# Optimization experiments

Hardware: AMD Instinct MI355X
Metric: run time of the kernel (lower is better)

Reference implementation:

```python
import jax, jax.numpy as jnp
import numpy as np

NUM_NODES = 50000
D_IN = 256
D_OUT = 256
N_QUERIES = 128
PER_GROUP = 256            # edges per query group in the last step (> max_edges)
E1 = N_QUERIES * PER_GROUP # 32768
E0 = 32768
RATIO = 0.2                # ratio_update


def setup_inputs() -> dict:
    key = jax.random.key(0)
    ks = jax.random.split(key, 10)
    d4 = 4 * D_IN
    rng = np.random.default_rng(0)
    # last-step edges: col0 = query idx (sorted, equal-size groups), col6 = src, col7 = dst
    edges1 = np.zeros((E1, 8), np.int64)
    edges1[:, 0] = np.repeat(np.arange(N_QUERIES), PER_GROUP)
    edges1[:, 6] = rng.integers(0, NUM_NODES, E1)
    edges1[:, 7] = rng.integers(0, NUM_NODES, E1)
    # earlier-step edges
    edges0 = np.zeros((E0, 8), np.int64)
    edges0[:, 0] = rng.integers(0, N_QUERIES, E0)
    edges0[:, 6] = rng.integers(0, NUM_NODES, E0)
    edges0[:, 7] = rng.integers(0, NUM_NODES, E0)
    return {
        "visited_node_score": jax.random.uniform(ks[0], (NUM_NODES,), jnp.float32),
        "visited_node_representation": jax.random.normal(ks[1], (NUM_NODES, D_IN), jnp.float32),
        "selected_edges0": jnp.asarray(edges0),
        "selected_edges1": jnp.asarray(edges1),
        "rel_emb0": jax.random.normal(ks[2], (E0, D_IN), jnp.float32),
        "rel_emb1": jax.random.normal(ks[3], (E1, D_IN), jnp.float32),
        "query_src_ts_emb": jax.random.normal(ks[4], (N_QUERIES, D_IN), jnp.float32),
        "query_rel_emb": jax.random.normal(ks[5], (N_QUERIES, D_IN), jnp.float32),
        "Wq": jax.random.normal(ks[6], (d4, d4), jnp.float32) * np.sqrt(2.0 / d4),
        "Wk": jax.random.normal(ks[7], (d4, d4), jnp.float32) * np.sqrt(2.0 / d4),
        "Wl": jax.random.normal(ks[8], (D_OUT, D_IN), jnp.float32) * np.sqrt(2.0 / (D_IN + D_OUT)),
        "bl": jnp.zeros((D_OUT,), jnp.float32),
        "max_edges": 64,
    }


def _att_score(edges, node_repr, rel, qst_tab, qr_tab, Wq, Wk):
    # G3: sum(Q(cat(vi,rel,qst,qr)) * K(cat(vj,rel,qst,qr)), -1) per edge
    q, src, dst = edges[:, 0], edges[:, 6], edges[:, 7]
    qst, qr = qst_tab[q], qr_tab[q]
    left = jnp.concatenate([node_repr[src], rel, qst, qr], axis=-1)   # [E, 4d]
    right = jnp.concatenate([node_repr[dst], rel, qst, qr], axis=-1)  # [E, 4d]
    return jnp.sum((left @ Wq.T) * (right @ Wk.T), axis=-1)          # [E]


def _seg_softmax(logits, seg, n):
    m = jax.ops.segment_max(logits, seg, num_segments=n)
    e = jnp.exp(logits - m[seg])
    s = jax.ops.segment_sum(e, seg, num_segments=n)
    return e / s[seg]


def _update_repr(edges, node_repr, w, ratio):
    # sparse mm: out[src] += (1-ratio)*w_e*repr[dst]; + identity for non-src rows, + ratio*repr for src rows
    src, dst = edges[:, 6], edges[:, 7]
    n = node_repr.shape[0]
    agg = jax.ops.segment_sum(((1.0 - ratio) * w)[:, None] * node_repr[dst], src, num_segments=n)
    is_src = jnp.zeros((n,), bool).at[src].set(True)
    diag = jnp.where(is_src, ratio, 1.0)
    return agg + diag[:, None] * node_repr


def reference(visited_node_score, visited_node_representation, selected_edges0,
              selected_edges1, rel_emb0, rel_emb1, query_src_ts_emb, query_rel_emb,
              Wq, Wk, Wl, bl, max_edges):
    n = visited_node_representation.shape[0]
    nq = query_src_ts_emb.shape[0]
    pg = selected_edges1.shape[0] // nq
    # attention on last step's edges
    logits = _att_score(selected_edges1, visited_node_representation, rel_emb1,
                        query_src_ts_emb, query_rel_emb, Wq, Wk)
    src1 = selected_edges1[:, 6]
    src_score = visited_node_score[src1]
    soft = _seg_softmax(logits, src1, n)
    target = soft * src_score
    # per-query-group top-k pruning (each group has pg > k edges)
    _, ti = jax.lax.top_k(target.reshape(nq, pg), max_edges)  # [nq, k]
    orig_indices = (ti + (jnp.arange(nq) * pg)[:, None]).reshape(-1)
    pruned_edges = selected_edges1[orig_indices]
    pruned_src_score = src_score[orig_indices]
    pruned_soft = soft[orig_indices]
    # sparse scatter-aggregation of scores onto dst (col 7)
    updated_node_score = jax.ops.segment_sum(pruned_soft * pruned_src_score,
                                             pruned_edges[:, 7], num_segments=n)
    node_repr = _update_repr(pruned_edges, visited_node_representation, pruned_soft, RATIO)
    # back-propagate representations through the earlier step
    tl = _att_score(selected_edges0, node_repr, rel_emb0, query_src_ts_emb, query_rel_emb, Wq, Wk)
    ts = _seg_softmax(tl, selected_edges0[:, 6], n)
    node_repr = _update_repr(selected_edges0, node_repr, ts, RATIO)
    # bypass_forward: LeakyReLU(Linear(.))
    node_repr = jax.nn.leaky_relu(node_repr @ Wl.T + bl)
    return (updated_node_score, node_repr, pruned_edges, orig_indices)
```

## Files before the change

kernel.cpp:

```cpp
#include <hip/hip_runtime.h>

#define NN 50000
#define D 256
#define NQ 128
#define PG 256
#define NE 32768
#define ME 64
#define BCAP 32
#define KDIM 256
#define NKT 8

typedef _Float16 f16;
typedef __attribute__((ext_vector_type(4))) _Float16 f16x4;
typedef __attribute__((ext_vector_type(8))) _Float16 f16x8;
typedef __attribute__((ext_vector_type(4))) float f32x4;

#define MFMA16(a,b,c) __builtin_amdgcn_mfma_f32_16x16x32_f16(a,b,c,0,0,0)

__device__ __forceinline__ f16x8 zero8(){
  f16x8 z;
#pragma unroll
  for (int i=0;i<8;++i) z[i] = (_Float16)0.f;
  return z;
}
__device__ __forceinline__ unsigned fenc(float f){
  unsigned b = __float_as_uint(f);
  return (b & 0x80000000u) ? ~b : (b | 0x80000000u);
}
__device__ __forceinline__ float fdec(unsigned u){
  unsigned b = (u & 0x80000000u) ? (u & 0x7fffffffu) : ~u;
  return __uint_as_float(b);
}

template<int EPI>
__global__ __launch_bounds__(256) void hgemm(const f16* __restrict__ Ah, const f16* __restrict__ Al,
                                             int Mrows,
                                             const f16* __restrict__ Bh, const f16* __restrict__ Bl,
                                             float* __restrict__ C, int ldc,
                                             const float* __restrict__ bias)
{
  __shared__ f16 AsH[128*40], AsL[128*40], BsH[128*40], BsL[128*40];
  const int tid = threadIdx.x;
  const int rb = blockIdx.x*128, cb = blockIdx.y*128;
  const int row = tid >> 1, ko = (tid & 1)*16;
  const bool aok = (rb + row) < Mrows;
  const int lane = tid & 63, wv = tid >> 6;
  const int qr = (wv & 1)*64, qc = (wv >> 1)*64;
  const int lm = lane & 15, qd = lane >> 4;

  const f16* gAh = Ah + (size_t)(rb+row)*KDIM + ko;
  const f16* gAl = Al + (size_t)(rb+row)*KDIM + ko;
  const f16* gBh = Bh + (size_t)(cb+row)*KDIM + ko;
  const f16* gBl = Bl + (size_t)(cb+row)*KDIM + ko;

  f16x8 pah0=zero8(), pah1=zero8(), pal0=zero8(), pal1=zero8();
  f16x8 pbh0, pbh1, pbl0, pbl1;
  if (aok){ pah0 = *(const f16x8*)gAh; pah1 = *(const f16x8*)(gAh+8);
            pal0 = *(const f16x8*)gAl; pal1 = *(const f16x8*)(gAl+8); }
  pbh0 = *(const f16x8*)gBh; pbh1 = *(const f16x8*)(gBh+8);
  pbl0 = *(const f16x8*)gBl; pbl1 = *(const f16x8*)(gBl+8);

  f32x4 acc[4][4];
#pragma unroll
  for (int t=0;t<4;++t)
#pragma unroll
    for (int u=0;u<4;++u)
#pragma unroll
      for (int r=0;r<4;++r) acc[t][u][r] = 0.f;

  const int wbase = row*40 + ko;
  for (int kt = 0; kt < NKT; ++kt){
    __syncthreads();
    *(f16x8*)(AsH + wbase) = pah0; *(f16x8*)(AsH + wbase + 8) = pah1;
    *(f16x8*)(AsL + wbase) = pal0; *(f16x8*)(AsL + wbase + 8) = pal1;
    *(f16x8*)(BsH + wbase) = pbh0; *(f16x8*)(BsH + wbase + 8) = pbh1;
    *(f16x8*)(BsL + wbase) = pbl0; *(f16x8*)(BsL + wbase + 8) = pbl1;
    __syncthreads();
    if (kt+1 < NKT){
      const int k0 = (kt+1)*32;
      if (aok){ pah0 = *(const f16x8*)(gAh + k0); pah1 = *(const f16x8*)(gAh + k0 + 8);
                pal0 = *(const f16x8*)(gAl + k0); pal1 = *(const f16x8*)(gAl + k0 + 8); }
      pbh0 = *(const f16x8*)(gBh + k0); pbh1 = *(const f16x8*)(gBh + k0 + 8);
      pbl0 = *(const f16x8*)(gBl + k0); pbl1 = *(const f16x8*)(gBl + k0 + 8);
    }
    f16x8 fah[4], fal[4], fbh[4], fbl[4];
#pragma unroll
    for (int t=0;t<4;++t){
      int off = (qr + t*16 + lm)*40 + qd*8;
      fah[t] = *(const f16x8*)(AsH + off);
      fal[t] = *(const f16x8*)(AsL + off);
    }
#pragma unroll
    for (int u=0;u<4;++u){
      int off = (qc + u*16 + lm)*40 + qd*8;
      fbh[u] = *(const f16x8*)(BsH + off);
      fbl[u] = *(const f16x8*)(BsL + off);
    }
#pragma unroll
    for (int t=0;t<4;++t)
#pragma unroll
      for (int u=0;u<4;++u){
        acc[t][u] = MFMA16(fah[t], fbh[u], acc[t][u]);
        acc[t][u] = MFMA16(fah[t], fbl[u], acc[t][u]);
        acc[t][u] = MFMA16(fal[t], fbh[u], acc[t][u]);
      }
  }
#pragma unroll
  for (int t=0;t<4;++t){
#pragma unroll
    for (int u=0;u<4;++u){
      int col = cb + qc + u*16 + lm;
      f32x4 v = acc[t][u];
#pragma unroll
      for (int r=0;r<4;++r){
        int rg = rb + qr + t*16 + qd*4 + r;
        if (rg < Mrows){
          float x = v[r];
          if (EPI==1){ x += bias[col]; x = x > 0.f ? x : 0.01f*x; }
          C[(size_t)rg*ldc + col] = x;
        }
      }
    }
  }
}

__global__ __launch_bounds__(256) void hgemm_rel(const f16* __restrict__ Ah, const f16* __restrict__ Al,
                                                 const f16* __restrict__ Bh, const f16* __restrict__ Bl,
                                                 const int* __restrict__ edges,
                                                 const float* __restrict__ H,
                                                 const float* __restrict__ Rel,
                                                 float* __restrict__ logits)
{
  __shared__ f16 AsH[128*40], AsL[128*40], BsH[128*40], BsL[128*40];
  __shared__ int sIdx[128];
  const int tid = threadIdx.x;
  const int rb = blockIdx.x*128, cb = blockIdx.y*128;
  const int sec = blockIdx.y >> 1;
  const int row = tid >> 1, ko = (tid & 1)*16;
  const int lane = tid & 63, wv = tid >> 6;
  const int qr = (wv & 1)*64, qc = (wv >> 1)*64;
  const int lm = lane & 15, qd = lane >> 4;

  if (tid < 128){
    int e = rb + tid;
    sIdx[tid] = (sec==0) ? edges[(size_t)e*8+6] : (sec==1 ? edges[(size_t)e*8+7] : 0);
  }

  const f16* gAh = Ah + (size_t)(rb+row)*KDIM + ko;
  const f16* gAl = Al + (size_t)(rb+row)*KDIM + ko;
  const f16* gBh = Bh + (size_t)(cb+row)*KDIM + ko;
  const f16* gBl = Bl + (size_t)(cb+row)*KDIM + ko;

  f16x8 pah0 = *(const f16x8*)gAh, pah1 = *(const f16x8*)(gAh+8);
  f16x8 pal0 = *(const f16x8*)gAl, pal1 = *(const f16x8*)(gAl+8);
  f16x8 pbh0 = *(const f16x8*)gBh, pbh1 = *(const f16x8*)(gBh+8);
  f16x8 pbl0 = *(const f16x8*)gBl, pbl1 = *(const f16x8*)(gBl+8);

  f32x4 acc[4][4];
#pragma unroll
  for (int t=0;t<4;++t)
#pragma unroll
    for (int u=0;u<4;++u)
#pragma unroll
      for (int r=0;r<4;++r) acc[t][u][r] = 0.f;

  const int wbase = row*40 + ko;
  for (int kt = 0; kt < NKT; ++kt){
    __syncthreads();
    *(f16x8*)(AsH + wbase) = pah0; *(f16x8*)(AsH + wbase + 8) = pah1;
    *(f16x8*)(AsL + wbase) = pal0; *(f16x8*)(AsL + wbase + 8) = pal1;
    *(f16x8*)(BsH + wbase) = pbh0; *(f16x8*)(BsH + wbase + 8) = pbh1;
    *(f16x8*)(BsL + wbase) = pbl0; *(f16x8*)(BsL + wbase + 8) = pbl1;
    __syncthreads();
    if (kt+1 < NKT){
      const int k0 = (kt+1)*32;
      pah0 = *(const f16x8*)(gAh + k0); pah1 = *(const f16x8*)(gAh + k0 + 8);
      pal0 = *(const f16x8*)(gAl + k0); pal1 = *(const f16x8*)(gAl + k0 + 8);
      pbh0 = *(const f16x8*)(gBh + k0); pbh1 = *(const f16x8*)(gBh + k0 + 8);
      pbl0 = *(const f16x8*)(gBl + k0); pbl1 = *(const f16x8*)(gBl + k0 + 8);
    }
    f16x8 fah[4], fal[4], fbh[4], fbl[4];
#pragma unroll
    for (int t=0;t<4;++t){
      int off = (qr + t*16 + lm)*40 + qd*8;
      fah[t] = *(const f16x8*)(AsH + off);
      fal[t] = *(const f16x8*)(AsL + off);
    }
#pragma unroll
    for (int u=0;u<4;++u){
      int off = (qc + u*16 + lm)*40 + qd*8;
      fbh[u] = *(const f16x8*)(BsH + off);
      fbl[u] = *(const f16x8*)(BsL + off);
    }
#pragma unroll
    for (int t=0;t<4;++t)
#pragma unroll
      for (int u=0;u<4;++u){
        acc[t][u] = MFMA16(fah[t], fbh[u], acc[t][u]);
        acc[t][u] = MFMA16(fah[t], fbl[u], acc[t][u]);
        acc[t][u] = MFMA16(fal[t], fbh[u], acc[t][u]);
      }
  }
  const int cbase = ((blockIdx.y & 1)*128) + qc + lm;
#pragma unroll
  for (int t=0;t<4;++t){
#pragma unroll
    for (int r=0;r<4;++r){
      int lrow = qr + t*16 + qd*4 + r;
      int e = rb + lrow;
      const float* xb = (sec==2) ? (Rel + (size_t)e*256)
                                 : (H + (size_t)sIdx[lrow]*256);
      float p = acc[t][0][r]*xb[cbase]
              + acc[t][1][r]*xb[cbase+16]
              + acc[t][2][r]*xb[cbase+32]
              + acc[t][3][r]*xb[cbase+48];
      p += __shfl_xor(p, 1); p += __shfl_xor(p, 2);
      p += __shfl_xor(p, 4); p += __shfl_xor(p, 8);
      if (lm == 0) atomicAdd(logits + e, p);
    }
  }
}

__global__ void split_f16(const float* __restrict__ X, f16* __restrict__ Xh,
                          f16* __restrict__ Xl, int n)
{
  int i = (blockIdx.x*256 + threadIdx.x)*4;
  if (i >= n) return;
  float4 v = *(const float4*)(X+i);
  f16x4 h, l;
  h[0]=(_Float16)v.x; h[1]=(_Float16)v.y; h[2]=(_Float16)v.z; h[3]=(_Float16)v.w;
  l[0]=(_Float16)(v.x-(float)h[0]); l[1]=(_Float16)(v.y-(float)h[1]);
  l[2]=(_Float16)(v.z-(float)h[2]); l[3]=(_Float16)(v.w-(float)h[3]);
  *(f16x4*)(Xh+i)=h; *(f16x4*)(Xl+i)=l;
}

__global__ void build_bt_mhh(const float* __restrict__ M, f16* __restrict__ Bh, f16* __restrict__ Bl)
{
  int idx = blockIdx.x*256 + threadIdx.x;
  int n = idx >> 8, k = idx & 255;
  float v = M[(size_t)k*1024 + n];
  _Float16 h = (_Float16)v;
  Bh[idx] = h; Bl[idx] = (_Float16)(v - (float)h);
}

__global__ void build_bt_wcat(const float* __restrict__ M, f16* __restrict__ Bh, f16* __restrict__ Bl)
{
  int idx = blockIdx.x*256 + threadIdx.x;
  int j = idx >> 8, k = idx & 255;
  float v;
  if (j < 256)      v = M[(size_t)j*1024 + 256 + k];
  else if (j < 512) v = M[(size_t)(256+k)*1024 + (j-256)];
  else              v = M[(size_t)(256 + j-512)*1024 + 256 + k];
  _Float16 h = (_Float16)v;
  Bh[idx] = h; Bl[idx] = (_Float16)(v - (float)h);
}

__global__ __launch_bounds__(256) void gemm_tn_split(const float* __restrict__ A,
                                                     const float* __restrict__ B,
                                                     double* __restrict__ Cpart)
{
  __shared__ float As[16][68];
  __shared__ float Bs[16][68];
  const int tid = threadIdx.x;
  const int rb = blockIdx.x * 64, cb = blockIdx.y * 64;
  const int z  = blockIdx.z;
  const int ty = tid >> 4, tx = tid & 15;
  const int aj = tid >> 4, akk = (tid & 15) << 2;
  double acc[4][4] = {};
  const int jbeg = z * 256, jend = jbeg + 256;
  for (int j0 = jbeg; j0 < jend; j0 += 16) {
    float4 av = *(const float4*)(A + (size_t)(j0+aj)*1024 + rb + akk);
    As[aj][akk+0]=av.x; As[aj][akk+1]=av.y; As[aj][akk+2]=av.z; As[aj][akk+3]=av.w;
    float4 bv = *(const float4*)(B + (size_t)(j0+aj)*1024 + cb + akk);
    Bs[aj][akk+0]=bv.x; Bs[aj][akk+1]=bv.y; Bs[aj][akk+2]=bv.z; Bs[aj][akk+3]=bv.w;
    __syncthreads();
#pragma unroll
    for (int jj=0; jj<16; ++jj){
      float a0=As[jj][ty*4+0],a1=As[jj][ty*4+1],a2=As[jj][ty*4+2],a3=As[jj][ty*4+3];
      float b0=Bs[jj][tx*4+0],b1=Bs[jj][tx*4+1],b2=Bs[jj][tx*4+2],b3=Bs[jj][tx*4+3];
      acc[0][0]+=(double)a0*b0; acc[0][1]+=(double)a0*b1; acc[0][2]+=(double)a0*b2; acc[0][3]+=(double)a0*b3;
      acc[1][0]+=(double)a1*b0; acc[1][1]+=(double)a1*b1; acc[1][2]+=(double)a1*b2; acc[1][3]+=(double)a1*b3;
      acc[2][0]+=(double)a2*b0; acc[2][1]+=(double)a2*b1; acc[2][2]+=(double)a2*b2; acc[2][3]+=(double)a2*b3;
      acc[3][0]+=(double)a3*b0; acc[3][1]+=(double)a3*b1; acc[3][2]+=(double)a3*b2; acc[3][3]+=(double)a3*b3;
    }
    __syncthreads();
  }
  double* Cz = Cpart + (size_t)z * 1048576;
#pragma unroll
  for (int i=0;i<4;++i)
#pragma unroll
    for (int j=0;j<4;++j)
      Cz[(size_t)(rb+ty*4+i)*1024 + cb+tx*4+j] = acc[i][j];
}

__global__ void reduce_m(const double* __restrict__ P, float* __restrict__ Mout)
{
  int i = blockIdx.x*256 + threadIdx.x;
  Mout[i] = (float)(P[i] + P[i+1048576] + P[i+2097152] + P[i+3145728]);
}

__global__ __launch_bounds__(256) void query_tables(const float* __restrict__ M,
    const float* __restrict__ qst, const float* __restrict__ qr,
    float* __restrict__ qt1, float* __restrict__ qt2, float* __restrict__ qw,
    float* __restrict__ qc)
{
  int q = blockIdx.x, t = threadIdx.x;
  __shared__ float g[512];
  __shared__ float red[256];
  g[t]       = qst[(size_t)q*256 + t];
  g[t + 256] = qr [(size_t)q*256 + t];
  __syncthreads();
  float s1=0.f, s2=0.f, sw=0.f, v1=0.f, v2=0.f;
  for (int k=0;k<512;++k){
    float gk = g[k];
    s1 += M[(size_t)t*1024 + 512 + k] * gk;
    s2 += M[(size_t)(512+k)*1024 + t] * gk;
    sw += (M[(size_t)(256+t)*1024 + 512 + k] +
           M[(size_t)(512+k)*1024 + 256 + t]) * gk;
    v1 += M[(size_t)(512+k)*1024 + 512 + t] * gk;
    v2 += M[(size_t)(512+k)*1024 + 768 + t] * gk;
  }
  qt1[(size_t)q*256+t]=s1; qt2[(size_t)q*256+t]=s2; qw[(size_t)q*256+t]=sw;
  red[t] = v1*g[t] + v2*g[t+256];
  __syncthreads();
  for (int s=128; s>0; s>>=1){
    if (t < s) red[t] += red[t+s];
    __syncthreads();
  }
  if (t==0) qc[q] = red[0];
}

__global__ __launch_bounds__(256) void slim_logits(const int* __restrict__ edges,
    const float* __restrict__ H, const float* __restrict__ U,
    const float* __restrict__ Rel,
    const float* __restrict__ qt1, const float* __restrict__ qt2,
    const float* __restrict__ qw, const float* __restrict__ qc,
    float* __restrict__ logits)
{
  int lane = threadIdx.x & 63;
  int e = blockIdx.x*4 + (threadIdx.x >> 6);
  int q   = edges[(size_t)e*8 + 0];
  int src = edges[(size_t)e*8 + 6];
  int dst = edges[(size_t)e*8 + 7];
  const float4* hs = (const float4*)(H   + (size_t)src*256);
  const float4* hd = (const float4*)(H   + (size_t)dst*256);
  const float4* us = (const float4*)(U   + (size_t)src*256);
  const float4* rl = (const float4*)(Rel + (size_t)e*256);
  const float4* t1 = (const float4*)(qt1 + (size_t)q*256);
  const float4* t2 = (const float4*)(qt2 + (size_t)q*256);
  const float4* w4 = (const float4*)(qw  + (size_t)q*256);
  float4 a, b, c;
  float s = 0.f;
  a = hd[lane]; b = us[lane]; c = t2[lane];
  s += a.x*(b.x+c.x) + a.y*(b.y+c.y) + a.z*(b.z+c.z) + a.w*(b.w+c.w);
  a = hs[lane]; c = t1[lane];
  s += a.x*c.x + a.y*c.y + a.z*c.z + a.w*c.w;
  a = rl[lane]; c = w4[lane];
  s += a.x*c.x + a.y*c.y + a.z*c.z + a.w*c.w;
#pragma unroll
  for (int off=32; off>0; off>>=1) s += __shfl_down(s, off);
  if (lane==0) logits[e] = s + qc[q];
}

__global__ void segmax_k(const int* __restrict__ edges, const float* __restrict__ logits,
                         unsigned* __restrict__ menc, int nE)
{
  int e = blockIdx.x*256 + threadIdx.x; if (e >= nE) return;
  atomicMax(menc + edges[(size_t)e*8+6], fenc(logits[e]));
}
__global__ void segexp_k(const int* __restrict__ edges, const float* __restrict__ logits,
                         const unsigned* __restrict__ menc, float* __restrict__ ebuf,
                         float* __restrict__ ssum, int nE)
{
  int e = blockIdx.x*256 + threadIdx.x; if (e >= nE) return;
  int s = edges[(size_t)e*8+6];
  float ex = expf(logits[e] - fdec(menc[s]));
  ebuf[e] = ex;
  atomicAdd(ssum + s, ex);
}
template<int TGT>
__global__ void segsoft_k(const int* __restrict__ edges, const float* __restrict__ ebuf,
                          const float* __restrict__ ssum, float* __restrict__ soft,
                          const float* __restrict__ score, float* __restrict__ target, int nE)
{
  int e = blockIdx.x*256 + threadIdx.x; if (e >= nE) return;
  int s = edges[(size_t)e*8+6];
  float so = ebuf[e] / ssum[s];
  soft[e] = so;
  if (TGT) target[e] = so * score[s];
}

__global__ __launch_bounds__(256) void topk_k(const float* __restrict__ target,
    const float* __restrict__ soft, const int* __restrict__ edges1,
    float* __restrict__ out0, float* __restrict__ out2, float* __restrict__ out3,
    int* __restrict__ p_src, int* __restrict__ p_dst, float* __restrict__ p_w)
{
  int qb = blockIdx.x, t = threadIdx.x;
  __shared__ float v[256];
  __shared__ int   ix[256];
  v[t] = target[(size_t)qb*256 + t];
  ix[t] = t;
  __syncthreads();
  for (int k=2; k<=256; k<<=1){
    for (int j=k>>1; j>0; j>>=1){
      int ixj = t ^ j;
      if (ixj > t){
        float va=v[t], vb=v[ixj]; int ia=ix[t], ib=ix[ixj];
        bool dir  = ((t & k) == 0);
        bool l_ab = (va > vb) || (va == vb && ia < ib);
        bool sw   = dir ? (!l_ab) : l_ab;
        if (sw){ v[t]=vb; v[ixj]=va; ix[t]=ib; ix[ixj]=ia; }
      }
      __syncthreads();
    }
  }
  if (t < 64){
    int oi = qb*256 + ix[t];
    int o  = qb*64 + t;
    out3[o] = (float)oi;
#pragma unroll
    for (int c2=0;c2<8;++c2) out2[(size_t)o*8 + c2] = (float)edges1[(size_t)oi*8 + c2];
    int s_ = edges1[(size_t)oi*8+6], d_ = edges1[(size_t)oi*8+7];
    p_src[o] = s_; p_dst[o] = d_; p_w[o] = soft[oi];
    atomicAdd(out0 + d_, v[t]);
  }
}

__global__ void bucket_fill(const int* __restrict__ srcarr, int stride, int n,
                            int* __restrict__ counts, int* __restrict__ bucket,
                            int* __restrict__ over, int* __restrict__ n_over)
{
  int e = blockIdx.x*256 + threadIdx.x; if (e >= n) return;
  int s = srcarr[(size_t)e*stride];
  int pos = atomicAdd(counts + s, 1);
  if (pos < BCAP) bucket[(size_t)s*BCAP + pos] = e;
  else { int oi = atomicAdd(n_over, 1); over[oi] = e; }
}

__global__ __launch_bounds__(256) void fused_update(const int* __restrict__ counts,
    const int* __restrict__ bucket, const int* __restrict__ dstarr, int dstride,
    const float* __restrict__ w, const float* __restrict__ Hin, float* __restrict__ Hout)
{
  int lane = threadIdx.x & 63;
  int n = blockIdx.x*4 + (threadIdx.x >> 6);
  if (n >= NN) return;
  int cnt = counts[n];
  float fac = cnt > 0 ? 0.2f : 1.0f;
  float4 h = ((const float4*)(Hin + (size_t)n*256))[lane];
  float4 acc = make_float4(fac*h.x, fac*h.y, fac*h.z, fac*h.w);
  int m = cnt < BCAP ? cnt : BCAP;
  for (int i=0;i<m;++i){
    int e = bucket[(size_t)n*BCAP + i];
    int d = dstarr[(size_t)e*dstride];
    float f = 0.8f * w[e];
    float4 vv = ((const float4*)(Hin + (size_t)d*256))[lane];
    acc.x += f*vv.x; acc.y += f*vv.y; acc.z += f*vv.z; acc.w += f*vv.w;
  }
  ((float4*)(Hout + (size_t)n*256))[lane] = acc;
}

__global__ __launch_bounds__(256) void over_k(const int* __restrict__ over,
    const int* __restrict__ n_over,
    const int* __restrict__ srcarr, int sstride,
    const int* __restrict__ dstarr, int dstride,
    const float* __restrict__ w, const float* __restrict__ Hin, float* __restrict__ Hout)
{
  int lane = threadIdx.x & 63;
  int i = blockIdx.x*4 + (threadIdx.x >> 6);
  if (i >= *n_over) return;
  int e = over[i];
  int s = srcarr[(size_t)e*sstride], d = dstarr[(size_t)e*dstride];
  float f = 0.8f * w[e];
  float4 vv = ((const float4*)(Hin + (size_t)d*256))[lane];
  float* o = Hout + (size_t)s*256 + lane*4;
  atomicAdd(o+0, f*vv.x); atomicAdd(o+1, f*vv.y);
  atomicAdd(o+2, f*vv.z); atomicAdd(o+3, f*vv.w);
}

extern "C" void kernel_launch(void* const* d_in, const int* in_sizes, int n_in,
                              void* d_out, int out_size, void* d_ws, size_t ws_size,
                              hipStream_t stream)
{
  const float* score = (const float*)d_in[0];
  const float* H0    = (const float*)d_in[1];
  const int*   edges0= (const int*)d_in[2];
  const int*   edges1= (const int*)d_in[3];
  const float* rel0  = (const float*)d_in[4];
  const float* rel1  = (const float*)d_in[5];
  const float* qst   = (const float*)d_in[6];
  const float* qr    = (const float*)d_in[7];
  const float* Wq    = (const float*)d_in[8];
  const float* Wk    = (const float*)d_in[9];
  const float* Wl    = (const float*)d_in[10];
  const float* bl    = (const float*)d_in[11];
  (void)in_sizes; (void)n_in; (void)out_size; (void)ws_size;

  float* out0 = (float*)d_out;
  float* out1 = out0 + NN;
  float* out2 = out1 + (size_t)NN*D;
  float* out3 = out2 + (size_t)NQ*ME*8;

  float* ws     = (float*)d_ws;
  float* Mbuf   = ws;
  float* qt1    = ws + 1048576;
  float* qt2    = ws + 1081344;
  float* qw     = ws + 1114112;
  float* qc     = ws + 1146880;
  float* logits = ws + 1147008;
  float* ebuf   = ws + 1179776;
  float* soft   = ws + 1212544;
  float* target = ws + 1245312;
  unsigned* menc= (unsigned*)(ws + 1278080);
  float* ssum   = ws + 1328080;
  int* p_src    = (int*)(ws + 1378080);
  int* p_dst    = (int*)(ws + 1386272);
  float* p_w    = ws + 1394464;
  float* U      = ws + 1402880;
  float* Hnew   = ws + 14202880;
  float* SCR    = ws + 27002880;
  int* counts = (int*)SCR;
  int* n_over = (int*)(SCR + 50000);
  int* over   = (int*)(SCR + 50056);
  int* bucket = (int*)(SCR + 100000);
  float* P0   = SCR + 2000000;
  f16* Ah = (f16*)P0;
  f16* Al = (f16*)(P0 + 6400000);
  f16* Rh = (f16*)(P0 + 12800000);
  f16* Rl = (f16*)(P0 + 16994304);
  f16* mhh_h  = (f16*)(P0 + 21200000);
  f16* mhh_l  = (f16*)(P0 + 21232768);
  f16* wcat_h = (f16*)(P0 + 21265536);
  f16* wcat_l = (f16*)(P0 + 21363840);
  f16* wl_h   = (f16*)(P0 + 21462144);
  f16* wl_l   = (f16*)(P0 + 21494912);
  double* Mpart = (double*)P0;
  float* Hpre = U;

  hipMemsetAsync(out0, 0, (size_t)NN*4, stream);
  hipMemsetAsync(menc, 0, (size_t)NN*4, stream);
  hipMemsetAsync(ssum, 0, (size_t)NN*4, stream);

  gemm_tn_split<<<dim3(16,16,4), 256, 0, stream>>>(Wq, Wk, Mpart);
  reduce_m<<<4096, 256, 0, stream>>>(Mpart, Mbuf);
  query_tables<<<NQ, 256, 0, stream>>>(Mbuf, qst, qr, qt1, qt2, qw, qc);
  build_bt_mhh<<<256, 256, 0, stream>>>(Mbuf, mhh_h, mhh_l);
  build_bt_wcat<<<768, 256, 0, stream>>>(Mbuf, wcat_h, wcat_l);
  split_f16<<<64, 256, 0, stream>>>(Wl, wl_h, wl_l, 65536);

  split_f16<<<12500, 256, 0, stream>>>(H0, Ah, Al, NN*256);
  hgemm<0><<<dim3(391,2), 256, 0, stream>>>(Ah, Al, NN, mhh_h, mhh_l, U, 256, nullptr);
  slim_logits<<<NE/4, 256, 0, stream>>>(edges1, H0, U, rel1, qt1, qt2, qw, qc, logits);
  split_f16<<<8192, 256, 0, stream>>>(rel1, Rh, Rl, NE*256);
  hgemm_rel<<<dim3(256,6), 256, 0, stream>>>(Rh, Rl, wcat_h, wcat_l, edges1, H0, rel1, logits);

  segmax_k<<<NE/256, 256, 0, stream>>>(edges1, logits, menc, NE);
  segexp_k<<<NE/256, 256, 0, stream>>>(edges1, logits, menc, ebuf, ssum, NE);
  segsoft_k<1><<<NE/256, 256, 0, stream>>>(edges1, ebuf, ssum, soft, score, target, NE);

  topk_k<<<NQ, 256, 0, stream>>>(target, soft, edges1, out0, out2, out3, p_src, p_dst, p_w);

  hipMemsetAsync(counts, 0, (size_t)NN*4, stream);
  hipMemsetAsync(n_over, 0, 4, stream);
  bucket_fill<<<(NQ*ME+255)/256, 256, 0, stream>>>(p_src, 1, NQ*ME, counts, bucket, over, n_over);
  fused_update<<<(NN+3)/4, 256, 0, stream>>>(counts, bucket, p_dst, 1, p_w, H0, Hnew);
  over_k<<<(NQ*ME)/4, 256, 0, stream>>>(over, n_over, p_src, 1, p_dst, 1, p_w, H0, Hnew);

  hipMemsetAsync(menc, 0, (size_t)NN*4, stream);
  hipMemsetAsync(ssum, 0, (size_t)NN*4, stream);

  split_f16<<<12500, 256, 0, stream>>>(Hnew, Ah, Al, NN*256);
  hgemm<0><<<dim3(391,2), 256, 0, stream>>>(Ah, Al, NN, mhh_h, mhh_l, U, 256, nullptr);
  slim_logits<<<NE/4, 256, 0, stream>>>(edges0, Hnew, U, rel0, qt1, qt2, qw, qc, logits);
  split_f16<<<8192, 256, 0, stream>>>(rel0, Rh, Rl, NE*256);
  hgemm_rel<<<dim3(256,6), 256, 0, stream>>>(Rh, Rl, wcat_h, wcat_l, edges0, Hnew, rel0, logits);

  segmax_k<<<NE/256, 256, 0, stream>>>(edges0, logits, menc, NE);
  segexp_k<<<NE/256, 256, 0, stream>>>(edges0, logits, menc, ebuf, ssum, NE);
  segsoft_k<0><<<NE/256, 256, 0, stream>>>(edges0, ebuf, ssum, soft, nullptr, nullptr, NE);

  hipMemsetAsync(counts, 0, (size_t)NN*4, stream);
  hipMemsetAsync(n_over, 0, 4, stream);
  bucket_fill<<<NE/256, 256, 0, stream>>>(edges0 + 6, 8, NE, counts, bucket, over, n_over);
  fused_update<<<(NN+3)/4, 256, 0, stream>>>(counts, bucket, edges0 + 7, 8, soft, Hnew, Hpre);
  over_k<<<NE/4, 256, 0, stream>>>(over, n_over, edges0 + 6, 8, edges0 + 7, 8, soft, Hnew, Hpre);

  split_f16<<<12500, 256, 0, stream>>>(Hpre, Ah, Al, NN*256);
  hgemm<1><<<dim3(391,2), 256, 0, stream>>>(Ah, Al, NN, wl_h, wl_l, out1, 256, bl);
}
```

Measured before the change: 739.2 us.

## Fuse f16 hi/lo split into GEMM loads and restructure query-table precompute

The GEMM kernels now read fp32 activations directly and split them into f16 high/low parts while staging into shared memory. This removes the five standalone split_f16 passes over the 50000x256 and 32768x256 matrices and their round trips through global memory. Separately, the per-query table computation moves from a serial 512-step loop per thread into a gather kernel plus a small tiled fp32 GEMM and a dot-product kernel. The Wq/Wk product split-K is widened from 4 to 8 partitions. The trade is extra conversion work inside the GEMM mainloop, twice the fp32 bytes per A load, and more small kernel launches.

```diff
diff --git a/kernel.cpp b/kernel.cpp
--- a/kernel.cpp
+++ b/kernel.cpp
@@ -17,12 +17,6 @@
 
 #define MFMA16(a,b,c) __builtin_amdgcn_mfma_f32_16x16x32_f16(a,b,c,0,0,0)
 
-__device__ __forceinline__ f16x8 zero8(){
-  f16x8 z;
-#pragma unroll
-  for (int i=0;i<8;++i) z[i] = (_Float16)0.f;
-  return z;
-}
 __device__ __forceinline__ unsigned fenc(float f){
   unsigned b = __float_as_uint(f);
   return (b & 0x80000000u) ? ~b : (b | 0x80000000u);
@@ -31,9 +25,18 @@
   unsigned b = (u & 0x80000000u) ? (u & 0x7fffffffu) : ~u;
   return __uint_as_float(b);
 }
+__device__ __forceinline__ void split8(float4 a, float4 b, f16x8& h, f16x8& l){
+  float v[8] = {a.x,a.y,a.z,a.w,b.x,b.y,b.z,b.w};
+#pragma unroll
+  for (int i=0;i<8;++i){
+    _Float16 hh = (_Float16)v[i];
+    h[i] = hh;
+    l[i] = (_Float16)(v[i] - (float)hh);
+  }
+}
 
 template<int EPI>
-__global__ __launch_bounds__(256) void hgemm(const f16* __restrict__ Ah, const f16* __restrict__ Al,
+__global__ __launch_bounds__(256) void hgemm(const float* __restrict__ A,
                                              int Mrows,
                                              const f16* __restrict__ Bh, const f16* __restrict__ Bl,
                                              float* __restrict__ C, int ldc,
@@ -45,18 +48,17 @@
   const int row = tid >> 1, ko = (tid & 1)*16;
   const bool aok = (rb + row) < Mrows;
   const int lane = tid & 63, wv = tid >> 6;
-  const int qr = (wv & 1)*64, qc = (wv >> 1)*64;
+  const int qrw = (wv & 1)*64, qcw = (wv >> 1)*64;
   const int lm = lane & 15, qd = lane >> 4;
 
-  const f16* gAh = Ah + (size_t)(rb+row)*KDIM + ko;
-  const f16* gAl = Al + (size_t)(rb+row)*KDIM + ko;
+  const float* gA = A + (size_t)(rb+row)*KDIM + ko;
   const f16* gBh = Bh + (size_t)(cb+row)*KDIM + ko;
   const f16* gBl = Bl + (size_t)(cb+row)*KDIM + ko;
 
-  f16x8 pah0=zero8(), pah1=zero8(), pal0=zero8(), pal1=zero8();
+  float4 pa0=make_float4(0.f,0.f,0.f,0.f), pa1=pa0, pa2=pa0, pa3=pa0;
   f16x8 pbh0, pbh1, pbl0, pbl1;
-  if (aok){ pah0 = *(const f16x8*)gAh; pah1 = *(const f16x8*)(gAh+8);
-            pal0 = *(const f16x8*)gAl; pal1 = *(const f16x8*)(gAl+8); }
+  if (aok){ pa0 = *(const float4*)gA;     pa1 = *(const float4*)(gA+4);
+            pa2 = *(const float4*)(gA+8); pa3 = *(const float4*)(gA+12); }
   pbh0 = *(const f16x8*)gBh; pbh1 = *(const f16x8*)(gBh+8);
   pbl0 = *(const f16x8*)gBl; pbl1 = *(const f16x8*)(gBl+8);
 
@@ -71,28 +73,32 @@
   const int wbase = row*40 + ko;
   for (int kt = 0; kt < NKT; ++kt){
     __syncthreads();
-    *(f16x8*)(AsH + wbase) = pah0; *(f16x8*)(AsH + wbase + 8) = pah1;
-    *(f16x8*)(AsL + wbase) = pal0; *(f16x8*)(AsL + wbase + 8) = pal1;
-    *(f16x8*)(BsH + wbase) = pbh0; *(f16x8*)(BsH + wbase + 8) = pbh1;
-    *(f16x8*)(BsL + wbase) = pbl0; *(f16x8*)(BsL + wbase + 8) = pbl1;
+    {
+      f16x8 h0,h1,l0,l1;
+      split8(pa0,pa1,h0,l0); split8(pa2,pa3,h1,l1);
+      *(f16x8*)(AsH + wbase) = h0; *(f16x8*)(AsH + wbase + 8) = h1;
+      *(f16x8*)(AsL + wbase) = l0; *(f16x8*)(AsL + wbase + 8) = l1;
+      *(f16x8*)(BsH + wbase) = pbh0; *(f16x8*)(BsH + wbase + 8) = pbh1;
+      *(f16x8*)(BsL + wbase) = pbl0; *(f16x8*)(BsL + wbase + 8) = pbl1;
+    }
     __syncthreads();
     if (kt+1 < NKT){
       const int k0 = (kt+1)*32;
-      if (aok){ pah0 = *(const f16x8*)(gAh + k0); pah1 = *(const f16x8*)(gAh + k0 + 8);
-                pal0 = *(const f16x8*)(gAl + k0); pal1 = *(const f16x8*)(gAl + k0 + 8); }
+      if (aok){ pa0 = *(const float4*)(gA + k0);     pa1 = *(const float4*)(gA + k0 + 4);
+                pa2 = *(const float4*)(gA + k0 + 8); pa3 = *(const float4*)(gA + k0 + 12); }
       pbh0 = *(const f16x8*)(gBh + k0); pbh1 = *(const f16x8*)(gBh + k0 + 8);
       pbl0 = *(const f16x8*)(gBl + k0); pbl1 = *(const f16x8*)(gBl + k0 + 8);
     }
     f16x8 fah[4], fal[4], fbh[4], fbl[4];
 #pragma unroll
     for (int t=0;t<4;++t){
-      int off = (qr + t*16 + lm)*40 + qd*8;
+      int off = (qrw + t*16 + lm)*40 + qd*8;
       fah[t] = *(const f16x8*)(AsH + off);
       fal[t] = *(const f16x8*)(AsL + off);
     }
 #pragma unroll
     for (int u=0;u<4;++u){
-      int off = (qc + u*16 + lm)*40 + qd*8;
+      int off = (qcw + u*16 + lm)*40 + qd*8;
       fbh[u] = *(const f16x8*)(BsH + off);
       fbl[u] = *(const f16x8*)(BsL + off);
     }
@@ -109,11 +115,11 @@
   for (int t=0;t<4;++t){
 #pragma unroll
     for (int u=0;u<4;++u){
-      int col = cb + qc + u*16 + lm;
+      int col = cb + qcw + u*16 + lm;
       f32x4 v = acc[t][u];
 #pragma unroll
       for (int r=0;r<4;++r){
-        int rg = rb + qr + t*16 + qd*4 + r;
+        int rg = rb + qrw + t*16 + qd*4 + r;
         if (rg < Mrows){
           float x = v[r];
           if (EPI==1){ x += bias[col]; x = x > 0.f ? x : 0.01f*x; }
@@ -124,7 +130,7 @@
   }
 }
 
-__global__ __launch_bounds__(256) void hgemm_rel(const f16* __restrict__ Ah, const f16* __restrict__ Al,
+__global__ __launch_bounds__(256) void hgemm_rel(const float* __restrict__ A,
                                                  const f16* __restrict__ Bh, const f16* __restrict__ Bl,
                                                  const int* __restrict__ edges,
                                                  const float* __restrict__ H,
@@ -138,7 +144,7 @@
   const int sec = blockIdx.y >> 1;
   const int row = tid >> 1, ko = (tid & 1)*16;
   const int lane = tid & 63, wv = tid >> 6;
-  const int qr = (wv & 1)*64, qc = (wv >> 1)*64;
+  const int qrw = (wv & 1)*64, qcw = (wv >> 1)*64;
   const int lm = lane & 15, qd = lane >> 4;
 
   if (tid < 128){
@@ -146,13 +152,12 @@
     sIdx[tid] = (sec==0) ? edges[(size_t)e*8+6] : (sec==1 ? edges[(size_t)e*8+7] : 0);
   }
 
-  const f16* gAh = Ah + (size_t)(rb+row)*KDIM + ko;
-  const f16* gAl = Al + (size_t)(rb+row)*KDIM + ko;
+  const float* gA = A + (size_t)(rb+row)*KDIM + ko;
   const f16* gBh = Bh + (size_t)(cb+row)*KDIM + ko;
   const f16* gBl = Bl + (size_t)(cb+row)*KDIM + ko;
 
-  f16x8 pah0 = *(const f16x8*)gAh, pah1 = *(const f16x8*)(gAh+8);
-  f16x8 pal0 = *(const f16x8*)gAl, pal1 = *(const f16x8*)(gAl+8);
+  float4 pa0 = *(const float4*)gA,     pa1 = *(const float4*)(gA+4);
+  float4 pa2 = *(const float4*)(gA+8), pa3 = *(const float4*)(gA+12);
   f16x8 pbh0 = *(const f16x8*)gBh, pbh1 = *(const f16x8*)(gBh+8);
   f16x8 pbl0 = *(const f16x8*)gBl, pbl1 = *(const f16x8*)(gBl+8);
 
@@ -167,28 +172,32 @@
   const int wbase = row*40 + ko;
   for (int kt = 0; kt < NKT; ++kt){
     __syncthreads();
-    *(f16x8*)(AsH + wbase) = pah0; *(f16x8*)(AsH + wbase + 8) = pah1;
-    *(f16x8*)(AsL + wbase) = pal0; *(f16x8*)(AsL + wbase + 8) = pal1;
-    *(f16x8*)(BsH + wbase) = pbh0; *(f16x8*)(BsH + wbase + 8) = pbh1;
-    *(f16x8*)(BsL + wbase) = pbl0; *(f16x8*)(BsL + wbase + 8) = pbl1;
+    {
+      f16x8 h0,h1,l0,l1;
+      split8(pa0,pa1,h0,l0); split8(pa2,pa3,h1,l1);
+      *(f16x8*)(AsH + wbase) = h0; *(f16x8*)(AsH + wbase + 8) = h1;
+      *(f16x8*)(AsL + wbase) = l0; *(f16x8*)(AsL + wbase + 8) = l1;
+      *(f16x8*)(BsH + wbase) = pbh0; *(f16x8*)(BsH + wbase + 8) = pbh1;
+      *(f16x8*)(BsL + wbase) = pbl0; *(f16x8*)(BsL + wbase + 8) = pbl1;
+    }
     __syncthreads();
     if (kt+1 < NKT){
       const int k0 = (kt+1)*32;
-      pah0 = *(const f16x8*)(gAh + k0); pah1 = *(const f16x8*)(gAh + k0 + 8);
-      pal0 = *(const f16x8*)(gAl + k0); pal1 = *(const f16x8*)(gAl + k0 + 8);
+      pa0 = *(const float4*)(gA + k0);     pa1 = *(const float4*)(gA + k0 + 4);
+      pa2 = *(const float4*)(gA + k0 + 8); pa3 = *(const float4*)(gA + k0 + 12);
       pbh0 = *(const f16x8*)(gBh + k0); pbh1 = *(const f16x8*)(gBh + k0 + 8);
       pbl0 = *(const f16x8*)(gBl + k0); pbl1 = *(const f16x8*)(gBl + k0 + 8);
     }
     f16x8 fah[4], fal[4], fbh[4], fbl[4];
 #pragma unroll
     for (int t=0;t<4;++t){
-      int off = (qr + t*16 + lm)*40 + qd*8;
+      int off = (qrw + t*16 + lm)*40 + qd*8;
       fah[t] = *(const f16x8*)(AsH + off);
       fal[t] = *(const f16x8*)(AsL + off);
     }
 #pragma unroll
     for (int u=0;u<4;++u){
-      int off = (qc + u*16 + lm)*40 + qd*8;
+      int off = (qcw + u*16 + lm)*40 + qd*8;
       fbh[u] = *(const f16x8*)(BsH + off);
       fbl[u] = *(const f16x8*)(BsL + off);
     }
@@ -201,12 +210,12 @@
         acc[t][u] = MFMA16(fal[t], fbh[u], acc[t][u]);
       }
   }
-  const int cbase = ((blockIdx.y & 1)*128) + qc + lm;
+  const int cbase = ((blockIdx.y & 1)*128) + qcw + lm;
 #pragma unroll
   for (int t=0;t<4;++t){
 #pragma unroll
     for (int r=0;r<4;++r){
-      int lrow = qr + t*16 + qd*4 + r;
+      int lrow = qrw + t*16 + qd*4 + r;
       int e = rb + lrow;
       const float* xb = (sec==2) ? (Rel + (size_t)e*256)
                                  : (H + (size_t)sIdx[lrow]*256);
@@ -267,7 +276,7 @@
   const int ty = tid >> 4, tx = tid & 15;
   const int aj = tid >> 4, akk = (tid & 15) << 2;
   double acc[4][4] = {};
-  const int jbeg = z * 256, jend = jbeg + 256;
+  const int jbeg = z * 128, jend = jbeg + 128;
   for (int j0 = jbeg; j0 < jend; j0 += 16) {
     float4 av = *(const float4*)(A + (size_t)(j0+aj)*1024 + rb + akk);
     As[aj][akk+0]=av.x; As[aj][akk+1]=av.y; As[aj][akk+2]=av.z; As[aj][akk+3]=av.w;
@@ -296,32 +305,95 @@
 __global__ void reduce_m(const double* __restrict__ P, float* __restrict__ Mout)
 {
   int i = blockIdx.x*256 + threadIdx.x;
-  Mout[i] = (float)(P[i] + P[i+1048576] + P[i+2097152] + P[i+3145728]);
-}
-
-__global__ __launch_bounds__(256) void query_tables(const float* __restrict__ M,
-    const float* __restrict__ qst, const float* __restrict__ qr,
-    float* __restrict__ qt1, float* __restrict__ qt2, float* __restrict__ qw,
-    float* __restrict__ qc)
-{
+  double s = 0.0;
+#pragma unroll
+  for (int z=0;z<8;++z) s += P[(size_t)i + (size_t)z*1048576];
+  Mout[i] = (float)s;
+}
+
+__global__ void build_g(const float* __restrict__ qst, const float* __restrict__ qr,
+                        float* __restrict__ G)
+{
+  int idx = blockIdx.x*256 + threadIdx.x;
+  int q = idx >> 9, k = idx & 511;
+  G[idx] = (k < 256) ? qst[(size_t)q*256 + k] : qr[(size_t)q*256 + k - 256];
+}
+
+__global__ void build_bq(const float* __restrict__ M, float* __restrict__ Bq)
+{
+  int idx = blockIdx.x*256 + threadIdx.x;
+  int k = idx / 1280, t = idx - k*1280;
+  float v;
+  if (t < 256)      v = M[(size_t)t*1024 + 512 + k];
+  else if (t < 512) v = M[(size_t)(512+k)*1024 + (t-256)];
+  else if (t < 768) v = M[(size_t)(256+(t-512))*1024 + 512 + k]
+                      + M[(size_t)(512+k)*1024 + 256 + (t-512)];
+  else              v = M[(size_t)(512+k)*1024 + 512 + (t-768)];
+  Bq[idx] = v;
+}
+
+__global__ __launch_bounds__(256) void gemm64(const float* __restrict__ A, int lda,
+                                              const float* __restrict__ B, int ldb,
+                                              float* __restrict__ C, int ldc,
+                                              int Mrows, int Kdim)
+{
+  __shared__ float As[16][68];
+  __shared__ float Bs[16][68];
+  const int tid = threadIdx.x;
+  const int rb = blockIdx.x*64, cb = blockIdx.y*64;
+  const int tx = tid & 15, ty = tid >> 4;
+  const int a_r = tid >> 2, a_k = (tid & 3)*4;
+  const int b_c = tid & 63, b_r0 = (tid >> 6)*4;
+  const bool aok = (rb + a_r) < Mrows;
+  float4 pa = make_float4(0.f,0.f,0.f,0.f);
+  float pb[4];
+  if (aok) pa = *(const float4*)(A + (size_t)(rb+a_r)*lda + a_k);
+#pragma unroll
+  for (int j=0;j<4;++j) pb[j] = B[(size_t)(b_r0+j)*ldb + cb + b_c];
+  float acc[4][4] = {};
+  const int NK = Kdim >> 4;
+  for (int t0=0; t0<NK; ++t0){
+    __syncthreads();
+    As[a_k+0][a_r]=pa.x; As[a_k+1][a_r]=pa.y; As[a_k+2][a_r]=pa.z; As[a_k+3][a_r]=pa.w;
+#pragma unroll
+    for (int j=0;j<4;++j) Bs[b_r0+j][b_c] = pb[j];
+    __syncthreads();
+    if (t0+1 < NK){
+      int k0 = (t0+1) << 4;
+      if (aok) pa = *(const float4*)(A + (size_t)(rb+a_r)*lda + k0 + a_k);
+#pragma unroll
+      for (int j=0;j<4;++j) pb[j] = B[(size_t)(k0+b_r0+j)*ldb + cb + b_c];
+    }
+#pragma unroll
+    for (int kk=0;kk<16;++kk){
+      float a[4], b[4];
+      *(float4*)&a[0] = *(const float4*)&As[kk][ty*4];
+#pragma unroll
+      for (int j=0;j<4;++j) b[j] = Bs[kk][tx + 16*j];
+#pragma unroll
+      for (int i=0;i<4;++i)
+#pragma unroll
+        for (int j=0;j<4;++j) acc[i][j] += a[i]*b[j];
+    }
+  }
+#pragma unroll
+  for (int i=0;i<4;++i){
+    int r = rb + ty*4 + i;
+    if (r < Mrows)
+#pragma unroll
+      for (int j=0;j<4;++j)
+        C[(size_t)r*ldc + cb + tx + 16*j] = acc[i][j];
+  }
+}
+
+__global__ __launch_bounds__(256) void qc_dot(const float* __restrict__ Ccat,
+    const float* __restrict__ qst, const float* __restrict__ qr, float* __restrict__ qc)
+{
+  __shared__ float red[256];
   int q = blockIdx.x, t = threadIdx.x;
-  __shared__ float g[512];
-  __shared__ float red[256];
-  g[t]       = qst[(size_t)q*256 + t];
-  g[t + 256] = qr [(size_t)q*256 + t];
-  __syncthreads();
-  float s1=0.f, s2=0.f, sw=0.f, v1=0.f, v2=0.f;
-  for (int k=0;k<512;++k){
-    float gk = g[k];
-    s1 += M[(size_t)t*1024 + 512 + k] * gk;
-    s2 += M[(size_t)(512+k)*1024 + t] * gk;
-    sw += (M[(size_t)(256+t)*1024 + 512 + k] +
-           M[(size_t)(512+k)*1024 + 256 + t]) * gk;
-    v1 += M[(size_t)(512+k)*1024 + 512 + t] * gk;
-    v2 += M[(size_t)(512+k)*1024 + 768 + t] * gk;
-  }
-  qt1[(size_t)q*256+t]=s1; qt2[(size_t)q*256+t]=s2; qw[(size_t)q*256+t]=sw;
-  red[t] = v1*g[t] + v2*g[t+256];
+  float a = Ccat[(size_t)q*1280 + 768 + t]  * qst[(size_t)q*256 + t]
+          + Ccat[(size_t)q*1280 + 1024 + t] * qr [(size_t)q*256 + t];
+  red[t] = a;
   __syncthreads();
   for (int s=128; s>0; s>>=1){
     if (t < s) red[t] += red[t+s];
@@ -333,8 +405,7 @@
 __global__ __launch_bounds__(256) void slim_logits(const int* __restrict__ edges,
     const float* __restrict__ H, const float* __restrict__ U,
     const float* __restrict__ Rel,
-    const float* __restrict__ qt1, const float* __restrict__ qt2,
-    const float* __restrict__ qw, const float* __restrict__ qc,
+    const float* __restrict__ Ct, const float* __restrict__ qc,
     float* __restrict__ logits)
 {
   int lane = threadIdx.x & 63;
@@ -346,9 +417,9 @@
   const float4* hd = (const float4*)(H   + (size_t)dst*256);
   const float4* us = (const float4*)(U   + (size_t)src*256);
   const float4* rl = (const float4*)(Rel + (size_t)e*256);
-  const float4* t1 = (const float4*)(qt1 + (size_t)q*256);
-  const float4* t2 = (const float4*)(qt2 + (size_t)q*256);
-  const float4* w4 = (const float4*)(qw  + (size_t)q*256);
+  const float4* t1 = (const float4*)(Ct + (size_t)q*1280);
+  const float4* t2 = (const float4*)(Ct + (size_t)q*1280 + 256);
+  const float4* w4 = (const float4*)(Ct + (size_t)q*1280 + 512);
   float4 a, b, c;
   float s = 0.f;
   a = hd[lane]; b = us[lane]; c = t2[lane];
@@ -502,56 +573,53 @@
 
   float* ws     = (float*)d_ws;
   float* Mbuf   = ws;
-  float* qt1    = ws + 1048576;
-  float* qt2    = ws + 1081344;
-  float* qw     = ws + 1114112;
-  float* qc     = ws + 1146880;
-  float* logits = ws + 1147008;
-  float* ebuf   = ws + 1179776;
-  float* soft   = ws + 1212544;
-  float* target = ws + 1245312;
-  unsigned* menc= (unsigned*)(ws + 1278080);
-  float* ssum   = ws + 1328080;
-  int* p_src    = (int*)(ws + 1378080);
-  int* p_dst    = (int*)(ws + 1386272);
-  float* p_w    = ws + 1394464;
-  float* U      = ws + 1402880;
-  float* Hnew   = ws + 14202880;
-  float* SCR    = ws + 27002880;
+  float* Ccat   = ws + 1048576;
+  float* qcv    = ws + 1212416;
+  float* G      = ws + 1212544;
+  float* logits = ws + 1278080;
+  float* ebuf   = ws + 1310848;
+  float* soft   = ws + 1343616;
+  float* target = ws + 1376384;
+  unsigned* menc= (unsigned*)(ws + 1409152);
+  float* ssum   = ws + 1459152;
+  int* p_src    = (int*)(ws + 1509152);
+  int* p_dst    = (int*)(ws + 1517344);
+  float* p_w    = ws + 1525536;
+  float* Bq     = ws + 1533728;
+  float* U      = ws + 2189088;
+  float* Hnew   = ws + 14989088;
+  float* SCR    = ws + 27789088;
   int* counts = (int*)SCR;
   int* n_over = (int*)(SCR + 50000);
   int* over   = (int*)(SCR + 50056);
   int* bucket = (int*)(SCR + 100000);
   float* P0   = SCR + 2000000;
-  f16* Ah = (f16*)P0;
-  f16* Al = (f16*)(P0 + 6400000);
-  f16* Rh = (f16*)(P0 + 12800000);
-  f16* Rl = (f16*)(P0 + 16994304);
-  f16* mhh_h  = (f16*)(P0 + 21200000);
-  f16* mhh_l  = (f16*)(P0 + 21232768);
-  f16* wcat_h = (f16*)(P0 + 21265536);
-  f16* wcat_l = (f16*)(P0 + 21363840);
-  f16* wl_h   = (f16*)(P0 + 21462144);
-  f16* wl_l   = (f16*)(P0 + 21494912);
   double* Mpart = (double*)P0;
+  f16* mhh_h  = (f16*)P0;
+  f16* mhh_l  = (f16*)(P0 + 32768);
+  f16* wcat_h = (f16*)(P0 + 65536);
+  f16* wcat_l = (f16*)(P0 + 163840);
+  f16* wl_h   = (f16*)(P0 + 262144);
+  f16* wl_l   = (f16*)(P0 + 294912);
   float* Hpre = U;
 
   hipMemsetAsync(out0, 0, (size_t)NN*4, stream);
   hipMemsetAsync(menc, 0, (size_t)NN*4, stream);
   hipMemsetAsync(ssum, 0, (size_t)NN*4, stream);
 
-  gemm_tn_split<<<dim3(16,16,4), 256, 0, stream>>>(Wq, Wk, Mpart);
+  gemm_tn_split<<<dim3(16,16,8), 256, 0, stream>>>(Wq, Wk, Mpart);
   reduce_m<<<4096, 256, 0, stream>>>(Mpart, Mbuf);
-  query_tables<<<NQ, 256, 0, stream>>>(Mbuf, qst, qr, qt1, qt2, qw, qc);
+  build_g<<<256, 256, 0, stream>>>(qst, qr, G);
+  build_bq<<<2560, 256, 0, stream>>>(Mbuf, Bq);
+  gemm64<<<dim3(2,20), 256, 0, stream>>>(G, 512, Bq, 1280, Ccat, 1280, NQ, 512);
+  qc_dot<<<NQ, 256, 0, stream>>>(Ccat, qst, qr, qcv);
   build_bt_mhh<<<256, 256, 0, stream>>>(Mbuf, mhh_h, mhh_l);
   build_bt_wcat<<<768, 256, 0, stream>>>(Mbuf, wcat_h, wcat_l);
   split_f16<<<64, 256, 0, stream>>>(Wl, wl_h, wl_l, 65536);
 
-  split_f16<<<12500, 256, 0, stream>>>(H0, Ah, Al, NN*256);
-  hgemm<0><<<dim3(391,2), 256, 0, stream>>>(Ah, Al, NN, mhh_h, mhh_l, U, 256, nullptr);
-  slim_logits<<<NE/4, 256, 0, stream>>>(edges1, H0, U, rel1, qt1, qt2, qw, qc, logits);
-  split_f16<<<8192, 256, 0, stream>>>(rel1, Rh, Rl, NE*256);
-  hgemm_rel<<<dim3(256,6), 256, 0, stream>>>(Rh, Rl, wcat_h, wcat_l, edges1, H0, rel1, logits);
+  hgemm<0><<<dim3(391,2), 256, 0, stream>>>(H0, NN, mhh_h, mhh_l, U, 256, nullptr);
+  slim_logits<<<NE/4, 256, 0, stream>>>(edges1, H0, U, rel1, Ccat, qcv, logits);
+  hgemm_rel<<<dim3(256,6), 256, 0, stream>>>(rel1, wcat_h, wcat_l, edges1, H0, rel1, logits);
 
   segmax_k<<<NE/256, 256, 0, stream>>>(edges1, logits, menc, NE);
   segexp_k<<<NE/256, 256, 0, stream>>>(edges1, logits, menc, ebuf, ssum, NE);
@@ -568,11 +636,9 @@
   hipMemsetAsync(menc, 0, (size_t)NN*4, stream);
   hipMemsetAsync(ssum, 0, (size_t)NN*4, stream);
 
-  split_f16<<<12500, 256, 0, stream>>>(Hnew, Ah, Al, NN*256);
-  hgemm<0><<<dim3(391,2), 256, 0, stream>>>(Ah, Al, NN, mhh_h, mhh_l, U, 256, nullptr);
-  slim_logits<<<NE/4, 256, 0, stream>>>(edges0, Hnew, U, rel0, qt1, qt2, qw, qc, logits);
-  split_f16<<<8192, 256, 0, stream>>>(rel0, Rh, Rl, NE*256);
-  hgemm_rel<<<dim3(256,6), 256, 0, stream>>>(Rh, Rl, wcat_h, wcat_l, edges0, Hnew, rel0, logits);
+  hgemm<0><<<dim3(391,2), 256, 0, stream>>>(Hnew, NN, mhh_h, mhh_l, U, 256, nullptr);
+  slim_logits<<<NE/4, 256, 0, stream>>>(edges0, Hnew, U, rel0, Ccat, qcv, logits);
+  hgemm_rel<<<dim3(256,6), 256, 0, stream>>>(rel0, wcat_h, wcat_l, edges0, Hnew, rel0, logits);
 
   segmax_k<<<NE/256, 256, 0, stream>>>(edges0, logits, menc, NE);
   segexp_k<<<NE/256, 256, 0, stream>>>(edges0, logits, menc, ebuf, ssum, NE);
@@ -584,6 +650,5 @@
   fused_update<<<(NN+3)/4, 256, 0, stream>>>(counts, bucket, edges0 + 7, 8, soft, Hnew, Hpre);
   over_k<<<NE/4, 256, 0, stream>>>(over, n_over, edges0 + 6, 8, edges0 + 7, 8, soft, Hnew, Hpre);
 
-  split_f16<<<12500, 256, 0, stream>>>(Hpre, Ah, Al, NN*256);
-  hgemm<1><<<dim3(391,2), 256, 0, stream>>>(Ah, Al, NN, wl_h, wl_l, out1, 256, bl);
-}
+  hgemm<1><<<dim3(391,2), 256, 0, stream>>>(Hpre, NN, wl_h, wl_l, out1, 256, bl);
+}
```

After: 631.2 us. 14.6% less time.
